# Kernel tuning notes

Hardware: AMD Instinct MI355X
Metric: run time of the kernel (lower is better)

## Reference

```python
import jax, jax.numpy as jnp
import numpy as np

N, K, DIN = 2, 2048, 1024
H, DOUT = 16, 64


def setup_inputs() -> dict:
    key = jax.random.key(0)
    ks = jax.random.split(key, 12)
    c_qk = float(np.sqrt(6.0 / (DIN + DOUT)))  # per-head q/k init scale
    c_v = c_qk  # dim_q == dim_v == DOUT here
    u = lambda k, shape, c: jax.random.uniform(k, shape, jnp.float32, -c, c)
    inp = {
        "query": jax.random.normal(ks[0], (N, K, DIN), jnp.float32),
        "key": jax.random.normal(ks[1], (N, K, DIN), jnp.float32),
        "value": jax.random.normal(ks[2], (N, K, DIN), jnp.float32),
        "mask": jax.random.randint(ks[3], (N, K, K), 0, 2) > 0,  # bool (N,K,K)
        # stacked per-head projection weights: (H, DIN, DOUT), biases (H, DOUT)
        "Wq": u(ks[4], (H, DIN, DOUT), c_qk),
        "bq": u(ks[5], (H, DOUT), c_qk),
        "Wk": u(ks[6], (H, DIN, DOUT), c_qk),
        "bk": u(ks[7], (H, DOUT), c_qk),
        "Wv": u(ks[8], (H, DIN, DOUT), c_v),
        "bv": u(ks[9], (H, DOUT), c_v),
        # output projection: (H*DOUT, DIN)
        "Wp": u(ks[10], (H * DOUT, DIN), c_qk),
        "bp": u(ks[11], (DIN,), c_qk),
    }
    return inp


def reference(query, key, value, mask, Wq, bq, Wk, bk, Wv, bv, Wp, bp):
    # Per-head projections, batched over heads: (N,K,DIN) x (H,DIN,DOUT) -> (N,H,K,DOUT)
    q = jnp.einsum("nkm,hmd->nhkd", query, Wq) + bq[None, :, None, :]
    k = jnp.einsum("nkm,hmd->nhkd", key, Wk) + bk[None, :, None, :]
    v = jnp.einsum("nkm,hmd->nhkd", value, Wv) + bv[None, :, None, :]
    # scaled dot-product scores: (N,H,K,K), scaled by sqrt(per-head dim)
    scores = jnp.einsum("nhkd,nhld->nhkl", q, k) / jnp.sqrt(jnp.asarray(DOUT, q.dtype))
    scores = jnp.where(mask[:, None, :, :], jnp.asarray(-1e9, scores.dtype), scores)
    w = jax.nn.softmax(scores, axis=-1)
    y = jnp.einsum("nhkl,nhld->nhkd", w, v)  # (N,H,K,DOUT)
    # concat heads along feature dim (head order matches torch cat over head list)
    y = jnp.transpose(y, (0, 2, 1, 3)).reshape(N, K, H * DOUT)
    return y @ Wp + bp
```

## Files before the change

kernel.cpp:

```cpp
#include <hip/hip_runtime.h>
#include <hip/hip_bf16.h>
#include <stdint.h>

typedef __attribute__((ext_vector_type(8))) __bf16 bf16x8;
typedef __attribute__((ext_vector_type(2))) __bf16 bf16x2;
typedef __attribute__((ext_vector_type(4))) float floatx4;

#define NB 2
#define SEQ 2048
#define DIN 1024
#define NH 16
#define DH 64
#define DMODEL 1024
#define BQ 128
#define BK 64
#define PAD 72
#define QSCALE 0.18033688011112042f

__device__ __forceinline__ float bf2f(unsigned short u) {
    return __uint_as_float(((unsigned)u) << 16);
}
__device__ __forceinline__ unsigned short f2bf(float f) {
    unsigned u = __float_as_uint(f);
    unsigned r = (u + 0x7FFFu + ((u >> 16) & 1u)) >> 16;
    return (unsigned short)r;
}
__device__ __forceinline__ float ldin(const void* p, size_t idx, int isbf) {
    return isbf ? bf2f(((const unsigned short*)p)[idx]) : ((const float*)p)[idx];
}

__device__ __forceinline__ void gl_lds16(const void* g, void* l) {
    __builtin_amdgcn_global_load_lds(
        reinterpret_cast<__attribute__((address_space(1))) unsigned int*>(
            reinterpret_cast<uintptr_t>(g)),
        reinterpret_cast<__attribute__((address_space(3))) unsigned int*>(
            reinterpret_cast<uintptr_t>(l)),
        16, 0, 0);
}

__device__ __forceinline__ int wave_is_bf16(const void* p) {
    unsigned short u = ((const unsigned short*)p)[2 * (threadIdx.x & 63)];
    int e = (u >> 7) & 0xFF;
    int sane = (u == 0 || (e > 100 && e < 140)) ? 1 : 0;
    return __popcll(__ballot(sane)) >= 32;
}
__device__ __forceinline__ int wave_mask_is_int(const void* p) {
    int v = ((const int*)p)[threadIdx.x & 63];
    int zo = (v == 0 || v == 1) ? 1 : 0;
    return __popcll(__ballot(zo)) >= 48;
}

__global__ __launch_bounds__(256) void prep(
    const void* __restrict__ q, const void* __restrict__ k, const void* __restrict__ v,
    const void* __restrict__ mask,
    const void* __restrict__ wq, const void* __restrict__ wk,
    const void* __restrict__ wv, const void* __restrict__ wp,
    unsigned short* __restrict__ a0, unsigned short* __restrict__ a1,
    unsigned short* __restrict__ a2,
    unsigned short* __restrict__ t0, unsigned short* __restrict__ t1,
    unsigned short* __restrict__ t2, unsigned short* __restrict__ t3,
    unsigned int* __restrict__ mbits)
{
    __shared__ float xls[64][68];
    const int b = blockIdx.x;
    const int tid = threadIdx.x;
    if (b < 12288) {
        int z = b >> 12, blk = b & 4095;
        const void* src = (z == 0) ? q : (z == 1) ? k : v;
        unsigned short* dst = (z == 0) ? a0 : (z == 1) ? a1 : a2;
        int isbf = wave_is_bf16(src);
        size_t i = ((size_t)blk * 256 + tid) * 4;
        if (isbf) {
            *(ushort4*)&dst[i] = *(const ushort4*)((const unsigned short*)src + i);
        } else {
            float4 f = *(const float4*)((const float*)src + i);
            ushort4 o;
            o.x = f2bf(f.x); o.y = f2bf(f.y); o.z = f2bf(f.z); o.w = f2bf(f.w);
            *(ushort4*)&dst[i] = o;
        }
    } else if (b < 13312) {
        int blk = b - 12288;
        int w = blk * 256 + tid;
        int is_int = wave_mask_is_int(mask);
        unsigned bits = 0;
        if (is_int) {
            const int4* p = (const int4*)mask + (size_t)w * 8;
#pragma unroll
            for (int g = 0; g < 8; ++g) {
                int4 vv = p[g];
                bits |= (unsigned)(vv.x != 0) << (g * 4 + 0);
                bits |= (unsigned)(vv.y != 0) << (g * 4 + 1);
                bits |= (unsigned)(vv.z != 0) << (g * 4 + 2);
                bits |= (unsigned)(vv.w != 0) << (g * 4 + 3);
            }
        } else {
            const uint4* p = (const uint4*)mask + (size_t)w * 2;
#pragma unroll
            for (int g = 0; g < 2; ++g) {
                uint4 vv = p[g];
                unsigned ws4[4] = {vv.x, vv.y, vv.z, vv.w};
#pragma unroll
                for (int c = 0; c < 4; ++c)
#pragma unroll
                    for (int bb = 0; bb < 4; ++bb)
                        bits |= (unsigned)(((ws4[c] >> (8 * bb)) & 0xFFu) != 0)
                                << (g * 16 + c * 4 + bb);
            }
        }
        mbits[w] = bits;
    } else {
        int zb = b - 13312;
        int z = zb >> 8, t = zb & 255;
        const void* src = (z == 0) ? wq : (z == 1) ? wk : (z == 2) ? wv : wp;
        unsigned short* dst = (z == 0) ? t0 : (z == 1) ? t1 : (z == 2) ? t2 : t3;
        int isbf = wave_is_bf16(src);
        int r = tid >> 2, cs = (tid & 3) * 16;
        if (z < 3) {
            int h = t >> 4, m0 = (t & 15) * 64;
#pragma unroll
            for (int j = 0; j < 16; ++j)
                xls[r][cs + j] = ldin(src, (size_t)h * 65536 + (size_t)(m0 + r) * 64 + cs + j, isbf);
            __syncthreads();
            int d2 = tid >> 2, ms = (tid & 3) * 16;
            size_t orow = (size_t)(h * 64 + d2) * 1024 + m0 + ms;
#pragma unroll
            for (int g = 0; g < 4; ++g) {
                ushort4 o;
                o.x = f2bf(xls[ms + g * 4 + 0][d2]);
                o.y = f2bf(xls[ms + g * 4 + 1][d2]);
                o.z = f2bf(xls[ms + g * 4 + 2][d2]);
                o.w = f2bf(xls[ms + g * 4 + 3][d2]);
                *(ushort4*)&dst[orow + g * 4] = o;
            }
        } else {
            int m0 = (t >> 4) * 64, c0 = (t & 15) * 64;
#pragma unroll
            for (int j = 0; j < 16; ++j)
                xls[r][cs + j] = ldin(src, (size_t)(m0 + r) * 1024 + c0 + cs + j, isbf);
            __syncthreads();
            int d2 = tid >> 2, ms = (tid & 3) * 16;
            size_t orow = (size_t)(c0 + d2) * 1024 + m0 + ms;
#pragma unroll
            for (int g = 0; g < 4; ++g) {
                ushort4 o;
                o.x = f2bf(xls[ms + g * 4 + 0][d2]);
                o.y = f2bf(xls[ms + g * 4 + 1][d2]);
                o.z = f2bf(xls[ms + g * 4 + 2][d2]);
                o.w = f2bf(xls[ms + g * 4 + 3][d2]);
                *(ushort4*)&dst[orow + g * 4] = o;
            }
        }
    }
}

__global__ __launch_bounds__(256) void gemm_mfma(
    const unsigned short* __restrict__ A0, const unsigned short* __restrict__ A1,
    const unsigned short* __restrict__ A2,
    const unsigned short* __restrict__ B0, const unsigned short* __restrict__ B1,
    const unsigned short* __restrict__ B2,
    const void* __restrict__ bias0, const void* __restrict__ bias1,
    const void* __restrict__ bias2,
    void* __restrict__ C0, void* __restrict__ C1, void* __restrict__ C2,
    int mode0)
{
    const int z = blockIdx.z;
    const unsigned short* A  = (z == 0) ? A0 : (z == 1) ? A1 : A2;
    const unsigned short* BT = (z == 0) ? B0 : (z == 1) ? B1 : B2;
    const void* bias = (z == 0) ? bias0 : (z == 1) ? bias1 : bias2;
    void* C = (z == 0) ? C0 : (z == 1) ? C1 : C2;
    const int mode = mode0 + z;
    const int isbf = wave_is_bf16(bias);
    const float scl = (mode == 0) ? QSCALE : 1.0f;

    const int lin  = blockIdx.x + (blockIdx.y << 3);
    const int xcd8 = lin & 7, loc = lin >> 3;
    const int n0   = (loc & 7) * 128;
    const int m0g  = ((xcd8 << 2) + (loc >> 3)) * 128;

    const int tid = threadIdx.x;
    const int wave = tid >> 6, lane = tid & 63;
    const int l16 = lane & 15, quad = lane >> 4;
    const int wm = wave & 1, wn = wave >> 1;

    __shared__ __align__(16) unsigned short smem[17408];
    unsigned short* As = smem;
    unsigned short* Bs = smem + 8192;

    floatx4 acc[4][4];
#pragma unroll
    for (int mt = 0; mt < 4; ++mt)
#pragma unroll
        for (int nt = 0; nt < 4; ++nt) acc[mt][nt] = floatx4{0.f, 0.f, 0.f, 0.f};

    const int lrow8 = lane >> 3;
    const int lseg  = (lane & 7) * 8;

    for (int kk = 0; kk < 1024; kk += 64) {
#pragma unroll
        for (int j = 0; j < 4; ++j) {
            int row0 = wave * 8 + j * 32;
            gl_lds16(&A[(size_t)(m0g + row0 + lrow8) * 1024 + kk + lseg], &As[row0 * 64]);
            gl_lds16(&BT[(size_t)(n0 + row0 + lrow8) * 1024 + kk + lseg], &Bs[row0 * 64]);
        }
        __syncthreads();
#pragma unroll
        for (int ks = 0; ks < 2; ++ks) {
            bf16x8 af[4], bf[4];
#pragma unroll
            for (int mt = 0; mt < 4; ++mt)
                af[mt] = *(const bf16x8*)&As[(wm * 64 + mt * 16 + l16) * 64 + ks * 32 + quad * 8];
#pragma unroll
            for (int nt = 0; nt < 4; ++nt)
                bf[nt] = *(const bf16x8*)&Bs[(wn * 64 + nt * 16 + l16) * 64 + ks * 32 + quad * 8];
#pragma unroll
            for (int mt = 0; mt < 4; ++mt)
#pragma unroll
                for (int nt = 0; nt < 4; ++nt)
                    acc[mt][nt] = __builtin_amdgcn_mfma_f32_16x16x32_bf16(af[mt], bf[nt], acc[mt][nt], 0, 0, 0);
        }
        __syncthreads();
    }

    float bv4[4];
#pragma unroll
    for (int nt = 0; nt < 4; ++nt)
        bv4[nt] = ldin(bias, n0 + wn * 64 + nt * 16 + l16, isbf);

    if (mode <= 1) {
        unsigned short* O = (unsigned short*)C;
#pragma unroll
        for (int mt = 0; mt < 4; ++mt)
#pragma unroll
            for (int reg = 0; reg < 4; ++reg) {
                int row = m0g + wm * 64 + mt * 16 + quad * 4 + reg;
                int nb = row >> 11, kq = row & (SEQ - 1);
#pragma unroll
                for (int nt = 0; nt < 4; ++nt) {
                    int c = n0 + wn * 64 + nt * 16 + l16;
                    int h = c >> 6, d = c & 63;
                    O[(((size_t)nb * NH + h) * SEQ + kq) * DH + d] =
                        f2bf((acc[mt][nt][reg] + bv4[nt]) * scl);
                }
            }
    } else if (mode == 2) {
#pragma unroll
        for (int mt = 0; mt < 4; ++mt)
#pragma unroll
            for (int nt = 0; nt < 4; ++nt)
#pragma unroll
                for (int reg = 0; reg < 4; ++reg) {
                    int m_l = wm * 64 + mt * 16 + quad * 4 + reg;
                    int c_l = wn * 64 + nt * 16 + l16;
                    smem[c_l * 136 + m_l] = f2bf(acc[mt][nt][reg] + bv4[nt]);
                }
        __syncthreads();
        unsigned short* O = (unsigned short*)C;
        int nb = m0g >> 11;
        int kq0 = m0g & (SEQ - 1);
#pragma unroll
        for (int j = 0; j < 8; ++j) {
            int i = tid + j * 256;
            int c_l = i >> 4, m8 = (i & 15) * 8;
            int cg = n0 + c_l, h = cg >> 6, d = cg & 63;
            *(bf16x8*)&O[(((size_t)nb * NH + h) * DH + d) * SEQ + kq0 + m8] =
                *(const bf16x8*)&smem[c_l * 136 + m8];
        }
    } else {
        unsigned short* Ob = (unsigned short*)C;
        float* Of = (float*)C;
#pragma unroll
        for (int mt = 0; mt < 4; ++mt)
#pragma unroll
            for (int reg = 0; reg < 4; ++reg) {
                int row = m0g + wm * 64 + mt * 16 + quad * 4 + reg;
#pragma unroll
                for (int nt = 0; nt < 4; ++nt) {
                    int c = n0 + wn * 64 + nt * 16 + l16;
                    float v = acc[mt][nt][reg] + bv4[nt];
                    if (isbf) Ob[(size_t)row * DMODEL + c] = f2bf(v);
                    else      Of[(size_t)row * DMODEL + c] = v;
                }
            }
    }
}

__global__ __launch_bounds__(512, 4) void attn_mfma(
    const unsigned short* __restrict__ qws, const unsigned short* __restrict__ kws,
    const unsigned short* __restrict__ vtws, const unsigned int* __restrict__ mbits,
    unsigned short* __restrict__ yws)
{
    const int linear = blockIdx.x + (blockIdx.y << 4) + (blockIdx.z << 8);
    const int xcd = linear & 7, loc = linear >> 3;
    const int hn  = (xcd << 2) + (loc >> 4);
    const int qt  = loc & 15;
    const int h   = hn & 15;
    const int n   = hn >> 4;

    const int tid  = threadIdx.x;
    const int wave = tid >> 6;
    const int lane = tid & 63;
    const int l16  = lane & 15;
    const int quad = lane >> 4;

    __shared__ __align__(16) unsigned short Ks[3][BK * DH];
    __shared__ __align__(16) unsigned short VTs[3][DH * BK];
    __shared__ __align__(16) unsigned short Ps[8][16 * PAD];

    const size_t base_nh = ((size_t)n * NH + h) * SEQ * DH;
    const size_t base_vt = ((size_t)n * NH + h) * DH * SEQ;
    const int q0 = qt * BQ;
    const int qrow = wave * 16 + l16;

    const unsigned int* mr0 = mbits + ((size_t)n * SEQ + q0 + qrow) * (SEQ / 32);
    bf16x8 af[2];
    {
        const unsigned short* qp = qws + base_nh + (size_t)(q0 + qrow) * DH + quad * 8;
        af[0] = *(const bf16x8*)qp;
        af[1] = *(const bf16x8*)(qp + 32);
    }

    const int srow8  = lane >> 3;
    const int schunk = ((lane & 7) ^ srow8) * 8;
    const int swz = l16 & 7;
    int koff[2], voff[2];
#pragma unroll
    for (int ks = 0; ks < 2; ++ks) {
        koff[ks] = l16 * DH + (((ks * 4 + quad) ^ swz) * 8);
        voff[ks] = l16 * BK + (((ks * 4 + quad) ^ swz) * 8);
    }

    bf16x8 vones;
#pragma unroll
    for (int j = 0; j < 8; ++j) vones[j] = (__bf16)1.0f;

    auto stage = [&](int b, int t) {
        int j0t = t * BK;
        int rl = wave * 8;
        gl_lds16(&kws[base_nh + (size_t)(j0t + rl + srow8) * DH + schunk], &Ks[b][rl * DH]);
        gl_lds16(&vtws[base_vt + (size_t)(rl + srow8) * SEQ + j0t + schunk], &VTs[b][rl * BK]);
    };

    floatx4 O[4];
#pragma unroll
    for (int dt = 0; dt < 4; ++dt) O[dt] = floatx4{0.f, 0.f, 0.f, 0.f};
    floatx4 Lacc = floatx4{0.f, 0.f, 0.f, 0.f};

    stage(0, 0);
    stage(1, 1);
    uint2 mwC = *(const uint2*)&mr0[0];
    uint2 mwN = *(const uint2*)&mr0[2];
    asm volatile("s_waitcnt vmcnt(0)" ::: "memory");
    __builtin_amdgcn_s_barrier();

    auto body = [&](int it, int cb, bool do_stage, int syncmode) {
        uint2 nA = {0, 0};
        if (do_stage) {
            int b2 = cb + 2; if (b2 >= 3) b2 -= 3;
            stage(b2, it + 2);
            nA = *(const uint2*)&mr0[(it + 2) * 2];
        }

        bf16x8 bfK[4][2];
#pragma unroll
        for (int nt = 0; nt < 4; ++nt)
#pragma unroll
            for (int ks = 0; ks < 2; ++ks)
                bfK[nt][ks] = *(const bf16x8*)&Ks[cb][nt * 16 * DH + koff[ks]];

        float St[4][4];
        __builtin_amdgcn_s_setprio(1);
#pragma unroll
        for (int nt = 0; nt < 4; ++nt) {
            floatx4 c = {0.f, 0.f, 0.f, 0.f};
            c = __builtin_amdgcn_mfma_f32_16x16x32_bf16(bfK[nt][0], af[0], c, 0, 0, 0);
            c = __builtin_amdgcn_mfma_f32_16x16x32_bf16(bfK[nt][1], af[1], c, 0, 0, 0);
            St[nt][0] = c[0]; St[nt][1] = c[1]; St[nt][2] = c[2]; St[nt][3] = c[3];
        }
        __builtin_amdgcn_s_setprio(0);

#pragma unroll
        for (int nt = 0; nt < 4; ++nt) {
            unsigned w = (nt & 2) ? mwC.y : mwC.x;
            int bb = (nt & 1) * 16 + quad * 4;
            float p[4];
#pragma unroll
            for (int r = 0; r < 4; ++r) {
                float e = __builtin_amdgcn_exp2f(St[nt][r]);
                p[r] = ((w >> (bb + r)) & 1u) ? 0.f : e;
            }
            bf16x2 e01, e23;
            e01[0] = (__bf16)p[0]; e01[1] = (__bf16)p[1];
            e23[0] = (__bf16)p[2]; e23[1] = (__bf16)p[3];
            uint2 pk;
            pk.x = *(unsigned*)&e01;
            pk.y = *(unsigned*)&e23;
            *(uint2*)&Ps[wave][l16 * PAD + nt * 16 + quad * 4] = pk;
        }

        bf16x8 pa[2], vb[4][2];
#pragma unroll
        for (int ks = 0; ks < 2; ++ks)
            pa[ks] = *(const bf16x8*)&Ps[wave][l16 * PAD + ks * 32 + quad * 8];
#pragma unroll
        for (int dt = 0; dt < 4; ++dt)
#pragma unroll
            for (int ks = 0; ks < 2; ++ks)
                vb[dt][ks] = *(const bf16x8*)&VTs[cb][dt * 16 * BK + voff[ks]];

        __builtin_amdgcn_s_setprio(1);
        Lacc = __builtin_amdgcn_mfma_f32_16x16x32_bf16(pa[0], vones, Lacc, 0, 0, 0);
        Lacc = __builtin_amdgcn_mfma_f32_16x16x32_bf16(pa[1], vones, Lacc, 0, 0, 0);
#pragma unroll
        for (int dt = 0; dt < 4; ++dt) {
            O[dt] = __builtin_amdgcn_mfma_f32_16x16x32_bf16(pa[0], vb[dt][0], O[dt], 0, 0, 0);
            O[dt] = __builtin_amdgcn_mfma_f32_16x16x32_bf16(pa[1], vb[dt][1], O[dt], 0, 0, 0);
        }
        __builtin_amdgcn_s_setprio(0);

        if (syncmode == 0) {
            asm volatile("s_waitcnt vmcnt(3)" ::: "memory");
            __builtin_amdgcn_s_barrier();
        } else if (syncmode == 1) {
            asm volatile("s_waitcnt vmcnt(0)" ::: "memory");
            __builtin_amdgcn_s_barrier();
        }
        mwC = mwN;
        mwN = nA;
    };

    for (int t3 = 0; t3 < 30; t3 += 3) {
        body(t3 + 0, 0, true, 0);
        body(t3 + 1, 1, true, 0);
        body(t3 + 2, 2, true, 0);
    }
    body(30, 0, false, 1);
    body(31, 1, false, 2);

#pragma unroll
    for (int r = 0; r < 4; ++r) {
        float lr = Lacc[r];
        float inv = (lr > 0.f) ? 1.f / lr : 0.f;
        int row = q0 + wave * 16 + quad * 4 + r;
#pragma unroll
        for (int dt = 0; dt < 4; ++dt) {
            int col = h * DH + dt * 16 + l16;
            yws[((size_t)n * SEQ + row) * DMODEL + col] = f2bf(O[dt][r] * inv);
        }
    }
}

extern "C" void kernel_launch(void* const* d_in, const int* in_sizes, int n_in,
                              void* d_out, int out_size, void* d_ws, size_t ws_size,
                              hipStream_t stream) {
    const void* query = d_in[0];
    const void* key_  = d_in[1];
    const void* value = d_in[2];
    const void* mask  = d_in[3];
    const void* Wq = d_in[4];
    const void* bq = d_in[5];
    const void* Wk = d_in[6];
    const void* bk = d_in[7];
    const void* Wv = d_in[8];
    const void* bv = d_in[9];
    const void* Wp = d_in[10];
    const void* bp = d_in[11];

    const size_t per = (size_t)NB * NH * SEQ * DH;
    unsigned short* us = (unsigned short*)d_ws;
    unsigned short* qws  = us;
    unsigned short* kws  = us + per;
    unsigned short* vtws = us + 2 * per;
    unsigned short* abf0 = us + 3 * per;
    unsigned short* abf1 = us + 4 * per;
    unsigned short* abf2 = us + 5 * per;
    unsigned short* wt0  = us + 6 * per;
    unsigned short* wt1  = wt0 + 1048576;
    unsigned short* wt2  = wt1 + 1048576;
    unsigned short* wt3  = wt2 + 1048576;
    unsigned int* mbits  = (unsigned int*)(wt3 + 1048576);
    unsigned short* yws = abf0;

    prep<<<dim3(14336), 256, 0, stream>>>(query, key_, value, mask,
                                          Wq, Wk, Wv, Wp,
                                          abf0, abf1, abf2,
                                          wt0, wt1, wt2, wt3, mbits);
    gemm_mfma<<<dim3(8, 32, 3), 256, 0, stream>>>(abf0, abf1, abf2, wt0, wt1, wt2,
                                                  bq, bk, bv, qws, kws, vtws, 0);
    attn_mfma<<<dim3(SEQ / BQ, NH, NB), 512, 0, stream>>>(qws, kws, vtws, mbits, yws);
    gemm_mfma<<<dim3(8, 32, 1), 256, 0, stream>>>(yws, yws, yws, wt3, wt3, wt3,
                                                  bp, bp, bp, d_out, d_out, d_out, 3);
}
```

Baseline: 279.3 us.

## Switch attention to double-buffered K/V staging and vectorize weight transpose loads

The attention kernel drops from a three-stage to a two-stage K/V LDS ring, prefetching one tile ahead instead of two, and raises the launch-bounds occupancy hint from 4 to 6. The aim is to cut LDS and register footprint so more workgroups fit per CU. In exchange there is less latency hiding, since each iteration now waits on vmcnt(0) before its barrier. Separately, the weight-transpose prep path now loads rows with float4/ushort4 vector loads instead of 16 scalar loads.

```diff
diff --git a/kernel.cpp b/kernel.cpp
--- a/kernel.cpp
+++ b/kernel.cpp
@@ -61,7 +61,7 @@
     unsigned short* __restrict__ t2, unsigned short* __restrict__ t3,
     unsigned int* __restrict__ mbits)
 {
-    __shared__ float xls[64][68];
+    __shared__ __align__(16) float xls[64][68];
     const int b = blockIdx.x;
     const int tid = threadIdx.x;
     if (b < 12288) {
@@ -115,40 +115,49 @@
         unsigned short* dst = (z == 0) ? t0 : (z == 1) ? t1 : (z == 2) ? t2 : t3;
         int isbf = wave_is_bf16(src);
         int r = tid >> 2, cs = (tid & 3) * 16;
+
+        size_t idx0;
         if (z < 3) {
-            int h = t >> 4, m0 = (t & 15) * 64;
-#pragma unroll
-            for (int j = 0; j < 16; ++j)
-                xls[r][cs + j] = ldin(src, (size_t)h * 65536 + (size_t)(m0 + r) * 64 + cs + j, isbf);
-            __syncthreads();
-            int d2 = tid >> 2, ms = (tid & 3) * 16;
-            size_t orow = (size_t)(h * 64 + d2) * 1024 + m0 + ms;
-#pragma unroll
-            for (int g = 0; g < 4; ++g) {
-                ushort4 o;
-                o.x = f2bf(xls[ms + g * 4 + 0][d2]);
-                o.y = f2bf(xls[ms + g * 4 + 1][d2]);
-                o.z = f2bf(xls[ms + g * 4 + 2][d2]);
-                o.w = f2bf(xls[ms + g * 4 + 3][d2]);
-                *(ushort4*)&dst[orow + g * 4] = o;
-            }
+            int hh = t >> 4, m0 = (t & 15) * 64;
+            idx0 = (size_t)hh * 65536 + (size_t)(m0 + r) * 64 + cs;
         } else {
             int m0 = (t >> 4) * 64, c0 = (t & 15) * 64;
-#pragma unroll
-            for (int j = 0; j < 16; ++j)
-                xls[r][cs + j] = ldin(src, (size_t)(m0 + r) * 1024 + c0 + cs + j, isbf);
-            __syncthreads();
-            int d2 = tid >> 2, ms = (tid & 3) * 16;
-            size_t orow = (size_t)(c0 + d2) * 1024 + m0 + ms;
+            idx0 = (size_t)(m0 + r) * 1024 + c0 + cs;
+        }
+        float4* xrow = (float4*)&xls[r][cs];
+        if (isbf) {
+            const unsigned short* sp = (const unsigned short*)src + idx0;
 #pragma unroll
             for (int g = 0; g < 4; ++g) {
-                ushort4 o;
-                o.x = f2bf(xls[ms + g * 4 + 0][d2]);
-                o.y = f2bf(xls[ms + g * 4 + 1][d2]);
-                o.z = f2bf(xls[ms + g * 4 + 2][d2]);
-                o.w = f2bf(xls[ms + g * 4 + 3][d2]);
-                *(ushort4*)&dst[orow + g * 4] = o;
-            }
+                ushort4 u = *(const ushort4*)(sp + g * 4);
+                float4 f;
+                f.x = bf2f(u.x); f.y = bf2f(u.y); f.z = bf2f(u.z); f.w = bf2f(u.w);
+                xrow[g] = f;
+            }
+        } else {
+            const float4* fp = (const float4*)((const float*)src + idx0);
+#pragma unroll
+            for (int g = 0; g < 4; ++g) xrow[g] = fp[g];
+        }
+        __syncthreads();
+
+        int d2 = tid >> 2, ms = (tid & 3) * 16;
+        size_t orow;
+        if (z < 3) {
+            int hh = t >> 4, m0 = (t & 15) * 64;
+            orow = (size_t)(hh * 64 + d2) * 1024 + m0 + ms;
+        } else {
+            int m0 = (t >> 4) * 64, c0 = (t & 15) * 64;
+            orow = (size_t)(c0 + d2) * 1024 + m0 + ms;
+        }
+#pragma unroll
+        for (int g = 0; g < 4; ++g) {
+            ushort4 o;
+            o.x = f2bf(xls[ms + g * 4 + 0][d2]);
+            o.y = f2bf(xls[ms + g * 4 + 1][d2]);
+            o.z = f2bf(xls[ms + g * 4 + 2][d2]);
+            o.w = f2bf(xls[ms + g * 4 + 3][d2]);
+            *(ushort4*)&dst[orow + g * 4] = o;
         }
     }
 }
@@ -284,7 +293,7 @@
     }
 }
 
-__global__ __launch_bounds__(512, 4) void attn_mfma(
+__global__ __launch_bounds__(512, 6) void attn_mfma(
     const unsigned short* __restrict__ qws, const unsigned short* __restrict__ kws,
     const unsigned short* __restrict__ vtws, const unsigned int* __restrict__ mbits,
     unsigned short* __restrict__ yws)
@@ -302,8 +311,8 @@
     const int l16  = lane & 15;
     const int quad = lane >> 4;
 
-    __shared__ __align__(16) unsigned short Ks[3][BK * DH];
-    __shared__ __align__(16) unsigned short VTs[3][DH * BK];
+    __shared__ __align__(16) unsigned short Ks[2][BK * DH];
+    __shared__ __align__(16) unsigned short VTs[2][DH * BK];
     __shared__ __align__(16) unsigned short Ps[8][16 * PAD];
 
     const size_t base_nh = ((size_t)n * NH + h) * SEQ * DH;
@@ -346,18 +355,15 @@
     floatx4 Lacc = floatx4{0.f, 0.f, 0.f, 0.f};
 
     stage(0, 0);
-    stage(1, 1);
     uint2 mwC = *(const uint2*)&mr0[0];
-    uint2 mwN = *(const uint2*)&mr0[2];
     asm volatile("s_waitcnt vmcnt(0)" ::: "memory");
     __builtin_amdgcn_s_barrier();
 
     auto body = [&](int it, int cb, bool do_stage, int syncmode) {
         uint2 nA = {0, 0};
         if (do_stage) {
-            int b2 = cb + 2; if (b2 >= 3) b2 -= 3;
-            stage(b2, it + 2);
-            nA = *(const uint2*)&mr0[(it + 2) * 2];
+            stage(cb ^ 1, it + 1);
+            nA = *(const uint2*)&mr0[(it + 1) * 2];
         }
 
         bf16x8 bfK[4][2];
@@ -418,22 +424,17 @@
         __builtin_amdgcn_s_setprio(0);
 
         if (syncmode == 0) {
-            asm volatile("s_waitcnt vmcnt(3)" ::: "memory");
-            __builtin_amdgcn_s_barrier();
-        } else if (syncmode == 1) {
             asm volatile("s_waitcnt vmcnt(0)" ::: "memory");
             __builtin_amdgcn_s_barrier();
         }
-        mwC = mwN;
-        mwN = nA;
+        mwC = nA;
     };
 
-    for (int t3 = 0; t3 < 30; t3 += 3) {
-        body(t3 + 0, 0, true, 0);
-        body(t3 + 1, 1, true, 0);
-        body(t3 + 2, 2, true, 0);
-    }
-    body(30, 0, false, 1);
+    for (int t2 = 0; t2 < 30; t2 += 2) {
+        body(t2 + 0, 0, true, 0);
+        body(t2 + 1, 1, true, 0);
+    }
+    body(30, 0, true, 0);
     body(31, 1, false, 2);
 
 #pragma unroll
```

Measured after the change: 423.3 us. +51.5%, slower.
